# Kernel optimization log

Measured on AMD Instinct MI355X. Metric: run time of the kernel, lower is better.

The kernel has to match this reference:

```python
import jax, jax.numpy as jnp
import numpy as np

T, HID, H, KV, D = 2048, 2048, 16, 8, 128
EPS = 1e-6
THETA = 10000.0


def setup_inputs() -> dict:
    key = jax.random.key(0)
    ks = jax.random.split(key, 4)
    return {
        "positions": jnp.arange(T, dtype=jnp.int32),
        "hidden_states": jax.random.normal(ks[0], (T, HID), dtype=jnp.float32),
        "layernorm_weight": jnp.ones((HID,), dtype=jnp.float32),
        "qkv_weight": jax.random.normal(ks[1], ((H + 2 * KV) * D, HID), dtype=jnp.float32) * 0.02,
        "q_norm_weight": jnp.ones((D,), dtype=jnp.float32),
        "k_norm_weight": jnp.ones((D,), dtype=jnp.float32),
        "o_weight": jax.random.normal(ks[2], (HID, H * D), dtype=jnp.float32) * 0.02,
    }


def _rms(x, w, eps=EPS):
    var = jnp.mean(jnp.square(x), axis=-1, keepdims=True)
    return x * jax.lax.rsqrt(var + eps) * w


def _rope(x, pos):
    # NeoX-style rotary over full head_dim. x: [T, nH, D]
    inv_freq = 1.0 / (THETA ** (jnp.arange(0, D, 2, dtype=jnp.float32) / D))
    ang = pos.astype(jnp.float32)[:, None] * inv_freq  # [T, D/2]
    cos, sin = jnp.cos(ang)[:, None, :], jnp.sin(ang)[:, None, :]
    x1, x2 = x[..., : D // 2], x[..., D // 2 :]
    return jnp.concatenate([x1 * cos - x2 * sin, x2 * cos + x1 * sin], axis=-1)


def reference(positions, hidden_states, layernorm_weight, qkv_weight,
              q_norm_weight, k_norm_weight, o_weight):
    # Fused RMSNorm + QKV projection
    normed = _rms(hidden_states, layernorm_weight)                 # [T, HID]
    qkv = normed @ qkv_weight.T                                    # [T, (H+2KV)*D]
    q, k, v = jnp.split(qkv, [H * D, (H + KV) * D], axis=-1)
    q = _rms(q.reshape(T, H, D), q_norm_weight)                    # per-head q norm
    k = _rms(k.reshape(T, KV, D), k_norm_weight)                   # per-head k norm
    v = v.reshape(T, KV, D)
    # RoPE
    q = _rope(q, positions)
    k = _rope(k, positions)
    # GQA causal attention
    scale = D ** -0.5
    kr = jnp.repeat(k, H // KV, axis=1)                            # [T, H, D]
    vr = jnp.repeat(v, H // KV, axis=1)
    scores = jnp.einsum("qhd,khd->hqk", q, kr) * scale             # [H, T, T]
    mask = jnp.tril(jnp.ones((T, T), dtype=bool))
    scores = jnp.where(mask[None], scores, jnp.finfo(scores.dtype).min)
    attn = jax.nn.softmax(scores, axis=-1)
    out = jnp.einsum("hqk,khd->qhd", attn, vr).reshape(T, H * D)
    return out @ o_weight.T                                        # [T, HID]
```

## Files before the change

kernel.cpp:

```cpp
#include <hip/hip_runtime.h>
#include <cstdint>
#include <cstddef>

typedef __bf16 bf16;
typedef __attribute__((ext_vector_type(8))) __bf16 bf16x8;
typedef __attribute__((ext_vector_type(4))) __bf16 bf16x4v;
typedef __attribute__((ext_vector_type(4))) float f32x4;
typedef __attribute__((ext_vector_type(4))) short short4v;

#define T_N   2048
#define HID_N 2048
#define NH    16
#define NKV   8
#define HD    128

#define MFMA(a, b, c) __builtin_amdgcn_mfma_f32_16x16x32_bf16((a), (b), (c), 0, 0, 0)

__device__ __forceinline__ f32x4 MFMA16(short4v a, short4v b, f32x4 c) {
#if __has_builtin(__builtin_amdgcn_mfma_f32_16x16x16bf16_1k)
    return __builtin_amdgcn_mfma_f32_16x16x16bf16_1k(a, b, c, 0, 0, 0);
#else
    asm volatile("v_mfma_f32_16x16x16_bf16 %0, %1, %2, %0\n\ts_nop 7\n\ts_nop 7"
                 : "+v"(c) : "v"(a), "v"(b));
    return c;
#endif
}

__device__ __forceinline__ void gl_lds16(const void* g, void* l) {
    __builtin_amdgcn_global_load_lds(
        (const __attribute__((address_space(1))) unsigned int*)g,
        (__attribute__((address_space(3))) unsigned int*)l,
        16, 0, 0);
}

__device__ __forceinline__ uint32_t pk2(float a, float b) {
    union { bf16 h; unsigned short u; } ca, cb;
    ca.h = (bf16)a; cb.h = (bf16)b;
    return ((uint32_t)cb.u << 16) | ca.u;
}

__global__ __launch_bounds__(256) void k_f2b(const float* __restrict__ in,
                                             bf16* __restrict__ out, int n) {
    int i = (blockIdx.x * 256 + threadIdx.x) * 8;
    if (i >= n) return;
    const float4* p = (const float4*)(in + i);
    float4 a = p[0], b = p[1];
    bf16x8 v;
    v[0] = (bf16)a.x; v[1] = (bf16)a.y; v[2] = (bf16)a.z; v[3] = (bf16)a.w;
    v[4] = (bf16)b.x; v[5] = (bf16)b.y; v[6] = (bf16)b.z; v[7] = (bf16)b.w;
    *(bf16x8*)(out + i) = v;
}

__global__ __launch_bounds__(256) void k_rmsnorm(const float* __restrict__ x,
                                                 const float* __restrict__ w,
                                                 bf16* __restrict__ out) {
    int row = blockIdx.x, tid = threadIdx.x;
    const float* xr = x + (size_t)row * HID_N;
    float4 a = ((const float4*)xr)[tid * 2];
    float4 b = ((const float4*)xr)[tid * 2 + 1];
    float ss = a.x*a.x + a.y*a.y + a.z*a.z + a.w*a.w
             + b.x*b.x + b.y*b.y + b.z*b.z + b.w*b.w;
    #pragma unroll
    for (int m = 32; m; m >>= 1) ss += __shfl_xor(ss, m);
    __shared__ float red[4];
    if ((tid & 63) == 0) red[tid >> 6] = ss;
    __syncthreads();
    float tot = red[0] + red[1] + red[2] + red[3];
    float rs = rsqrtf(tot * (1.0f / HID_N) + 1e-6f);
    const float4* wr = (const float4*)(w + tid * 8);
    float4 wa = wr[0], wb = wr[1];
    bf16x8 v;
    v[0] = (bf16)(a.x * rs * wa.x); v[1] = (bf16)(a.y * rs * wa.y);
    v[2] = (bf16)(a.z * rs * wa.z); v[3] = (bf16)(a.w * rs * wa.w);
    v[4] = (bf16)(b.x * rs * wb.x); v[5] = (bf16)(b.y * rs * wb.y);
    v[6] = (bf16)(b.z * rs * wb.z); v[7] = (bf16)(b.w * rs * wb.w);
    *(bf16x8*)(out + (size_t)row * HID_N + tid * 8) = v;
}

__global__ __launch_bounds__(256, 2) void k_gemm_bt(const bf16* __restrict__ A,
                                                    const bf16* __restrict__ B,
                                                    float* __restrict__ C,
                                                    int M, int N, int K) {
    __shared__ __attribute__((aligned(16))) bf16 As[128 * 64];
    __shared__ __attribute__((aligned(16))) bf16 Bs[128 * 64];
    const int tid = threadIdx.x;
    const int lane = tid & 63, wid = tid >> 6;
    const int wm = wid >> 1, wn = wid & 1;
    const int r = lane & 15, g = lane >> 4;
    const size_t bm = (size_t)blockIdx.y * 128, bn = (size_t)blockIdx.x * 128;

    f32x4 acc[4][4] = {};

    const int srow = tid >> 3;
    const int schk = tid & 7;

    for (int k0 = 0; k0 < K; k0 += 64) {
        __syncthreads();
        #pragma unroll
        for (int c = 0; c < 4; c++) {
            int row = c * 32 + srow;
            int ka = (schk ^ (row & 7)) << 3;
            gl_lds16(A + (bm + row) * (size_t)K + k0 + ka,
                     (char*)As + c * 4096 + tid * 16);
            gl_lds16(B + (bn + row) * (size_t)K + k0 + ka,
                     (char*)Bs + c * 4096 + tid * 16);
        }
        __syncthreads();
        #pragma unroll
        for (int kk = 0; kk < 2; kk++) {
            bf16x8 af[4], bfr[4];
            #pragma unroll
            for (int m = 0; m < 4; m++) {
                int row = wm * 64 + m * 16 + r;
                af[m] = *(const bf16x8*)(As + row * 64 + (((kk * 4 + g) ^ (row & 7)) << 3));
            }
            #pragma unroll
            for (int n = 0; n < 4; n++) {
                int row = wn * 64 + n * 16 + r;
                bfr[n] = *(const bf16x8*)(Bs + row * 64 + (((kk * 4 + g) ^ (row & 7)) << 3));
            }
            #pragma unroll
            for (int m = 0; m < 4; m++)
                #pragma unroll
                for (int n = 0; n < 4; n++)
                    acc[m][n] = MFMA(af[m], bfr[n], acc[m][n]);
        }
    }
    #pragma unroll
    for (int m = 0; m < 4; m++)
        #pragma unroll
        for (int n = 0; n < 4; n++)
            #pragma unroll
            for (int j = 0; j < 4; j++) {
                size_t row = bm + wm * 64 + m * 16 + g * 4 + j;
                size_t col = bn + wn * 64 + n * 16 + r;
                C[row * (size_t)N + col] = acc[m][n][j];
            }
}

__global__ __launch_bounds__(128) void k_normrope(const float* __restrict__ qkv,
                                                  const float* __restrict__ qw,
                                                  const float* __restrict__ kw,
                                                  const int* __restrict__ pos,
                                                  bf16* __restrict__ q,
                                                  bf16* __restrict__ k,
                                                  bf16* __restrict__ v) {
    int t = blockIdx.x, hs = blockIdx.y, d = threadIdx.x;
    const float* base = qkv + (size_t)t * 4096;
    if (hs >= 24) {
        int hv = hs - 24;
        v[((size_t)t * NKV + hv) * HD + d] = (bf16)base[3072 + hv * 128 + d];
        return;
    }
    bool isq = hs < 16;
    int h = isq ? hs : hs - 16;
    float x = isq ? base[h * 128 + d] : base[2048 + h * 128 + d];
    float ss = x * x;
    #pragma unroll
    for (int m = 32; m; m >>= 1) ss += __shfl_xor(ss, m);
    __shared__ float red[2];
    if ((d & 63) == 0) red[d >> 6] = ss;
    __syncthreads();
    float rs = rsqrtf((red[0] + red[1]) * (1.0f / HD) + 1e-6f);
    float nx = x * rs * (isq ? qw[d] : kw[d]);
    __shared__ float sh[128];
    sh[d] = nx;
    __syncthreads();
    float other = sh[d ^ 64];
    int j = d & 63;
    float ang = (float)pos[t] * __powf(10000.f, -(float)j * (1.f / 64.f));
    float s, c;
    __sincosf(ang, &s, &c);
    float o = (d < 64) ? (nx * c - other * s) : (nx * c + other * s);
    bf16* dst = isq ? (q + ((size_t)t * NH + h) * HD + d)
                    : (k + ((size_t)t * NKV + h) * HD + d);
    *dst = (bf16)o;
}

__global__ __launch_bounds__(256, 3) void k_flash(const bf16* __restrict__ Q,
                                                  const bf16* __restrict__ K,
                                                  const bf16* __restrict__ V,
                                                  bf16* __restrict__ On,
                                                  float* __restrict__ ml) {
    __shared__ __attribute__((aligned(16))) bf16 Ks2[2][64 * 128];
    __shared__ __attribute__((aligned(16))) bf16 Vt[128 * 64];

    const int tid = threadIdx.x, lane = tid & 63, w = tid >> 6;
    const int r = lane & 15, g = lane >> 4;
    const int h = blockIdx.x, y = blockIdx.y;
    int ci, qt;
    if (y < 32)      { ci = 0; qt = y; }
    else if (y < 56) { ci = 1; qt = y - 24; }
    else if (y < 72) { ci = 2; qt = y - 40; }
    else             { ci = 3; qt = y - 48; }
    const int c0 = ci * 8;
    const int ntl = min(qt + 1 - c0, 8);
    const int q0 = qt * 64;
    const int gh = h >> 1;
    const int q0w = q0 + w * 16;

    const int rowk = tid >> 4, posc = tid & 15;
    const int vd = tid & 127, vhalf = tid >> 7;

    bf16x8 qf[4];
    #pragma unroll
    for (int ks = 0; ks < 4; ks++)
        qf[ks] = *(const bf16x8*)(Q + ((size_t)(q0w + r) * NH + h) * HD + ks * 32 + g * 8);

    f32x4 acc[8] = {};
    float m_run = -1e30f, l_run = 0.f;
    const float scale = 0.08838834764831845f;

    {
        const int kv0 = c0 * 64;
        #pragma unroll
        for (int c = 0; c < 4; c++) {
            int row = c * 16 + rowk;
            int srcc = posc ^ (row & 7);
            gl_lds16(K + ((size_t)(kv0 + row) * NKV + gh) * HD + srcc * 8,
                     (char*)&Ks2[0][0] + c * 4096 + tid * 16);
        }
        bf16x8 vr[4];
        #pragma unroll
        for (int it = 0; it < 4; it++) {
            int kb = vhalf + it * 2;
            const bf16* src = V + ((size_t)(kv0 + kb * 8) * NKV + gh) * HD + vd;
            #pragma unroll
            for (int i = 0; i < 8; i++) vr[it][i] = src[(size_t)i * (NKV * HD)];
        }
        #pragma unroll
        for (int it = 0; it < 4; it++) {
            int kb = vhalf + it * 2;
            *(bf16x8*)(&Vt[0] + vd * 64 + ((kb ^ (vd & 7)) * 8)) = vr[it];
        }
        __syncthreads();
    }

    for (int t = 0; t < ntl; ++t) {
        const int b = t & 1;
        const int kv0 = (c0 + t) * 64;
        const bool pf = (t + 1 < ntl);
        bf16x8 vr[4];
        if (pf) {
            const int kv1 = kv0 + 64;
            #pragma unroll
            for (int c = 0; c < 4; c++) {
                int row = c * 16 + rowk;
                int srcc = posc ^ (row & 7);
                gl_lds16(K + ((size_t)(kv1 + row) * NKV + gh) * HD + srcc * 8,
                         (char*)&Ks2[0][0] + (b ^ 1) * 16384 + c * 4096 + tid * 16);
            }
            #pragma unroll
            for (int it = 0; it < 4; it++) {
                int kb = vhalf + it * 2;
                const bf16* src = V + ((size_t)(kv1 + kb * 8) * NKV + gh) * HD + vd;
                #pragma unroll
                for (int i = 0; i < 8; i++) vr[it][i] = src[(size_t)i * (NKV * HD)];
            }
        }
        if (kv0 <= q0w + 15) {
            const bf16* Kb = &Ks2[b][0];
            const char* Vb = (const char*)&Vt[0];
            float sc[4][4];
            __builtin_amdgcn_s_setprio(1);
            #pragma unroll
            for (int t4 = 0; t4 < 4; t4++) {
                f32x4 S = {};
                #pragma unroll
                for (int ks = 0; ks < 4; ks++) {
                    int row = t4 * 16 + r;
                    bf16x8 kf = *(const bf16x8*)(Kb + row * 128 + (((4 * ks + g) ^ (row & 7)) * 8));
                    S = MFMA(kf, qf[ks], S);
                }
                #pragma unroll
                for (int j = 0; j < 4; j++) {
                    int kg = kv0 + t4 * 16 + 4 * g + j;
                    sc[t4][j] = (kg <= q0w + r) ? S[j] * scale : -1e30f;
                }
            }
            __builtin_amdgcn_s_setprio(0);
            float mx = sc[0][0];
            #pragma unroll
            for (int t4 = 0; t4 < 4; t4++)
                #pragma unroll
                for (int j = 0; j < 4; j++) mx = fmaxf(mx, sc[t4][j]);
            mx = fmaxf(mx, __shfl_xor(mx, 16));
            mx = fmaxf(mx, __shfl_xor(mx, 32));
            float mn = fmaxf(m_run, mx);
            float alpha = __expf(m_run - mn);
            m_run = mn;
            float rsum = 0.f;
            #pragma unroll
            for (int t4 = 0; t4 < 4; t4++)
                #pragma unroll
                for (int j = 0; j < 4; j++) {
                    sc[t4][j] = __expf(sc[t4][j] - mn);
                    rsum += sc[t4][j];
                }
            rsum += __shfl_xor(rsum, 16);
            rsum += __shfl_xor(rsum, 32);
            l_run = l_run * alpha + rsum;
            #pragma unroll
            for (int f = 0; f < 8; f++)
                #pragma unroll
                for (int j = 0; j < 4; j++) acc[f][j] *= alpha;
            union PB { uint32_t u[2]; short4v s; };
            PB pbu[4];
            #pragma unroll
            for (int t4 = 0; t4 < 4; t4++) {
                pbu[t4].u[0] = pk2(sc[t4][0], sc[t4][1]);
                pbu[t4].u[1] = pk2(sc[t4][2], sc[t4][3]);
            }
            __builtin_amdgcn_s_setprio(1);
            #pragma unroll
            for (int f = 0; f < 8; f++) {
                #pragma unroll
                for (int t4 = 0; t4 < 4; t4++) {
                    short4v vf = *(const short4v*)(Vb + f * 2048 + r * 128 +
                                  (((2 * t4 + (g >> 1)) ^ (r & 7)) * 16) + (g & 1) * 8);
                    acc[f] = MFMA16(vf, pbu[t4].s, acc[f]);
                }
            }
            __builtin_amdgcn_s_setprio(0);
        }
        if (pf) {
            __syncthreads();
            #pragma unroll
            for (int it = 0; it < 4; it++) {
                int kb = vhalf + it * 2;
                *(bf16x8*)(&Vt[0] + vd * 64 + ((kb ^ (vd & 7)) * 8)) = vr[it];
            }
            __syncthreads();
        }
    }
    const int lr = w * 16 + r;
    float inv_l = 1.0f / l_run;
    bf16* Ob = On + ((size_t)(h * 80 + y)) * 8192 + lr * 128;
    #pragma unroll
    for (int f = 0; f < 8; f++) {
        bf16x4v ov;
        #pragma unroll
        for (int j = 0; j < 4; j++) ov[j] = (bf16)(acc[f][j] * inv_l);
        *(bf16x4v*)(Ob + f * 16 + 4 * g) = ov;
    }
    if (g == 0) {
        float* mlp = ml + ((size_t)(h * 80 + y)) * 128;
        mlp[lr] = m_run;
        mlp[64 + lr] = l_run;
    }
}

__global__ __launch_bounds__(256) void k_comb(const bf16* __restrict__ On,
                                              const float* __restrict__ ml,
                                              bf16* __restrict__ ao) {
    const int h = blockIdx.x, qt = blockIdx.y;
    const int lr = threadIdx.x & 63, db = threadIdx.x >> 6;
    const int nc = 1 + (qt >= 8) + (qt >= 16) + (qt >= 24);
    const int ys[4] = {qt, qt + 24, qt + 40, qt + 48};
    float mi[4], li[4], wi[4];
    float mstar = -1e30f;
    for (int i = 0; i < 4; i++) {
        if (i < nc) {
            const float* p = ml + ((size_t)(h * 80 + ys[i])) * 128;
            mi[i] = p[lr]; li[i] = p[64 + lr];
            mstar = fmaxf(mstar, mi[i]);
        }
    }
    float wsum = 0.f;
    for (int i = 0; i < 4; i++) {
        if (i < nc) { wi[i] = li[i] * __expf(mi[i] - mstar); wsum += wi[i]; }
        else wi[i] = 0.f;
    }
    float inv = 1.f / wsum;
    for (int i = 0; i < 4; i++) wi[i] *= inv;
    const int q = qt * 64 + lr;
    #pragma unroll
    for (int dd = 0; dd < 4; dd++) {
        int d0 = db * 32 + dd * 8;
        float o[8] = {};
        for (int i = 0; i < 4; i++) {
            if (i < nc) {
                bf16x8 v = *(const bf16x8*)(On + ((size_t)(h * 80 + ys[i])) * 8192 + lr * 128 + d0);
                #pragma unroll
                for (int j = 0; j < 8; j++) o[j] += wi[i] * (float)v[j];
            }
        }
        bf16x8 ov;
        #pragma unroll
        for (int j = 0; j < 8; j++) ov[j] = (bf16)o[j];
        *(bf16x8*)(ao + ((size_t)q * NH + h) * HD + d0) = ov;
    }
}

extern "C" void kernel_launch(void* const* d_in, const int* in_sizes, int n_in,
                              void* d_out, int out_size, void* d_ws, size_t ws_size,
                              hipStream_t stream) {
    const int*   pos  = (const int*)d_in[0];
    const float* hid  = (const float*)d_in[1];
    const float* lw   = (const float*)d_in[2];
    const float* qkvw = (const float*)d_in[3];
    const float* qnw  = (const float*)d_in[4];
    const float* knw  = (const float*)d_in[5];
    const float* ow   = (const float*)d_in[6];
    float* out = (float*)d_out;

    char* ws = (char*)d_ws;
    bf16*  qkvw_b = (bf16*)(ws);
    bf16*  ow_b   = (bf16*)(ws + (16u << 20));
    bf16*  normed = (bf16*)(ws + (24u << 20));
    float* qkvf   = (float*)(ws + (32u << 20));
    bf16*  qb     = (bf16*)(ws + (64u << 20));
    bf16*  kb     = (bf16*)(ws + (72u << 20));
    bf16*  vb     = (bf16*)(ws + (76u << 20));
    bf16*  ao     = normed;
    bf16*  On     = (bf16*)(ws + (32u << 20));
    float* ml     = (float*)(ws + (54u << 20));

    k_f2b<<<4096, 256, 0, stream>>>(qkvw, qkvw_b, 4096 * 2048);
    k_f2b<<<2048, 256, 0, stream>>>(ow, ow_b, 2048 * 2048);
    k_rmsnorm<<<T_N, 256, 0, stream>>>(hid, lw, normed);
    k_gemm_bt<<<dim3(32, 16), 256, 0, stream>>>(normed, qkvw_b, qkvf, 2048, 4096, 2048);
    k_normrope<<<dim3(T_N, 32), 128, 0, stream>>>(qkvf, qnw, knw, pos, qb, kb, vb);
    k_flash<<<dim3(NH, 80), 256, 0, stream>>>(qb, kb, vb, On, ml);
    k_comb<<<dim3(NH, 32), 256, 0, stream>>>(On, ml, ao);
    k_gemm_bt<<<dim3(16, 16), 256, 0, stream>>>(ao, ow_b, out, 2048, 2048, 2048);
}
```

Before: 185.7 us.

## Emit bf16 QKV from GEMM, write V directly, skip masking and lazy rescale in flash

A dedicated QKV GEMM writes its output as bf16 and stores the V columns directly into the V buffer. This removes the fp32 intermediate and the V copy pass, and k_normrope now handles two heads per 256-thread block. The flash kernel skips causal masking on tiles that are fully below the diagonal. It also skips the online-softmax rescale when the new max exceeds the running max by no more than 8, which bounds exp values by e^8 and so trades a small accuracy risk for fewer multiplies. GEMM launch bounds are raised to 3 blocks per CU, which may force register spills.

Measured after the change: 185.1 us. Within noise of the previous version (-0.4%).

```diff
diff --git a/kernel.cpp b/kernel.cpp
--- a/kernel.cpp
+++ b/kernel.cpp
@@ -77,7 +77,7 @@
     *(bf16x8*)(out + (size_t)row * HID_N + tid * 8) = v;
 }
 
-__global__ __launch_bounds__(256, 2) void k_gemm_bt(const bf16* __restrict__ A,
+__global__ __launch_bounds__(256, 3) void k_gemm_bt(const bf16* __restrict__ A,
                                                     const bf16* __restrict__ B,
                                                     float* __restrict__ C,
                                                     int M, int N, int K) {
@@ -138,35 +138,93 @@
             }
 }
 
-__global__ __launch_bounds__(128) void k_normrope(const float* __restrict__ qkv,
+__global__ __launch_bounds__(256, 3) void k_gemm_qkv(const bf16* __restrict__ A,
+                                                     const bf16* __restrict__ B,
+                                                     bf16* __restrict__ qkv3,
+                                                     bf16* __restrict__ vb) {
+    const int K = HID_N;
+    __shared__ __attribute__((aligned(16))) bf16 As[128 * 64];
+    __shared__ __attribute__((aligned(16))) bf16 Bs[128 * 64];
+    const int tid = threadIdx.x;
+    const int lane = tid & 63, wid = tid >> 6;
+    const int wm = wid >> 1, wn = wid & 1;
+    const int r = lane & 15, g = lane >> 4;
+    const size_t bm = (size_t)blockIdx.y * 128, bn = (size_t)blockIdx.x * 128;
+
+    f32x4 acc[4][4] = {};
+    const int srow = tid >> 3;
+    const int schk = tid & 7;
+
+    for (int k0 = 0; k0 < K; k0 += 64) {
+        __syncthreads();
+        #pragma unroll
+        for (int c = 0; c < 4; c++) {
+            int row = c * 32 + srow;
+            int ka = (schk ^ (row & 7)) << 3;
+            gl_lds16(A + (bm + row) * (size_t)K + k0 + ka,
+                     (char*)As + c * 4096 + tid * 16);
+            gl_lds16(B + (bn + row) * (size_t)K + k0 + ka,
+                     (char*)Bs + c * 4096 + tid * 16);
+        }
+        __syncthreads();
+        #pragma unroll
+        for (int kk = 0; kk < 2; kk++) {
+            bf16x8 af[4], bfr[4];
+            #pragma unroll
+            for (int m = 0; m < 4; m++) {
+                int row = wm * 64 + m * 16 + r;
+                af[m] = *(const bf16x8*)(As + row * 64 + (((kk * 4 + g) ^ (row & 7)) << 3));
+            }
+            #pragma unroll
+            for (int n = 0; n < 4; n++) {
+                int row = wn * 64 + n * 16 + r;
+                bfr[n] = *(const bf16x8*)(Bs + row * 64 + (((kk * 4 + g) ^ (row & 7)) << 3));
+            }
+            #pragma unroll
+            for (int m = 0; m < 4; m++)
+                #pragma unroll
+                for (int n = 0; n < 4; n++)
+                    acc[m][n] = MFMA(af[m], bfr[n], acc[m][n]);
+        }
+    }
+    #pragma unroll
+    for (int m = 0; m < 4; m++)
+        #pragma unroll
+        for (int n = 0; n < 4; n++)
+            #pragma unroll
+            for (int j = 0; j < 4; j++) {
+                size_t row = bm + wm * 64 + m * 16 + g * 4 + j;
+                size_t col = bn + wn * 64 + n * 16 + r;
+                bf16 val = (bf16)acc[m][n][j];
+                if (col < 3072) qkv3[row * 3072 + col] = val;
+                else            vb[row * 1024 + (col - 3072)] = val;
+            }
+}
+
+__global__ __launch_bounds__(256) void k_normrope(const bf16* __restrict__ qkv3,
                                                   const float* __restrict__ qw,
                                                   const float* __restrict__ kw,
                                                   const int* __restrict__ pos,
                                                   bf16* __restrict__ q,
-                                                  bf16* __restrict__ k,
-                                                  bf16* __restrict__ v) {
-    int t = blockIdx.x, hs = blockIdx.y, d = threadIdx.x;
-    const float* base = qkv + (size_t)t * 4096;
-    if (hs >= 24) {
-        int hv = hs - 24;
-        v[((size_t)t * NKV + hv) * HD + d] = (bf16)base[3072 + hv * 128 + d];
-        return;
-    }
-    bool isq = hs < 16;
-    int h = isq ? hs : hs - 16;
-    float x = isq ? base[h * 128 + d] : base[2048 + h * 128 + d];
+                                                  bf16* __restrict__ k) {
+    const int t = blockIdx.x, tid = threadIdx.x;
+    const int half = tid >> 7, d = tid & 127;
+    const int slot = blockIdx.y * 2 + half;
+    const bool isq = slot < 16;
+    const int h = isq ? slot : slot - 16;
+    float x = (float)qkv3[(size_t)t * 3072 + slot * 128 + d];
     float ss = x * x;
     #pragma unroll
     for (int m = 32; m; m >>= 1) ss += __shfl_xor(ss, m);
-    __shared__ float red[2];
-    if ((d & 63) == 0) red[d >> 6] = ss;
+    __shared__ float red[4];
+    __shared__ float sh[256];
+    if ((tid & 63) == 0) red[tid >> 6] = ss;
     __syncthreads();
-    float rs = rsqrtf((red[0] + red[1]) * (1.0f / HD) + 1e-6f);
+    float rs = rsqrtf((red[half * 2] + red[half * 2 + 1]) * (1.0f / HD) + 1e-6f);
     float nx = x * rs * (isq ? qw[d] : kw[d]);
-    __shared__ float sh[128];
-    sh[d] = nx;
+    sh[tid] = nx;
     __syncthreads();
-    float other = sh[d ^ 64];
+    float other = sh[tid ^ 64];
     int j = d & 63;
     float ang = (float)pos[t] * __powf(10000.f, -(float)j * (1.f / 64.f));
     float s, c;
@@ -261,6 +319,7 @@
         if (kv0 <= q0w + 15) {
             const bf16* Kb = &Ks2[b][0];
             const char* Vb = (const char*)&Vt[0];
+            const bool fullt = (kv0 + 63 <= q0w);
             float sc[4][4];
             __builtin_amdgcn_s_setprio(1);
             #pragma unroll
@@ -272,10 +331,15 @@
                     bf16x8 kf = *(const bf16x8*)(Kb + row * 128 + (((4 * ks + g) ^ (row & 7)) * 8));
                     S = MFMA(kf, qf[ks], S);
                 }
-                #pragma unroll
-                for (int j = 0; j < 4; j++) {
-                    int kg = kv0 + t4 * 16 + 4 * g + j;
-                    sc[t4][j] = (kg <= q0w + r) ? S[j] * scale : -1e30f;
+                if (fullt) {
+                    #pragma unroll
+                    for (int j = 0; j < 4; j++) sc[t4][j] = S[j] * scale;
+                } else {
+                    #pragma unroll
+                    for (int j = 0; j < 4; j++) {
+                        int kg = kv0 + t4 * 16 + 4 * g + j;
+                        sc[t4][j] = (kg <= q0w + r) ? S[j] * scale : -1e30f;
+                    }
                 }
             }
             __builtin_amdgcn_s_setprio(0);
@@ -286,9 +350,10 @@
                 for (int j = 0; j < 4; j++) mx = fmaxf(mx, sc[t4][j]);
             mx = fmaxf(mx, __shfl_xor(mx, 16));
             mx = fmaxf(mx, __shfl_xor(mx, 32));
-            float mn = fmaxf(m_run, mx);
-            float alpha = __expf(m_run - mn);
-            m_run = mn;
+            const bool nr = __all(mx <= m_run + 8.0f) != 0;
+            float mn, alpha;
+            if (nr) { mn = m_run; alpha = 1.0f; }
+            else    { mn = fmaxf(m_run, mx); alpha = __expf(m_run - mn); m_run = mn; }
             float rsum = 0.f;
             #pragma unroll
             for (int t4 = 0; t4 < 4; t4++)
@@ -300,10 +365,12 @@
             rsum += __shfl_xor(rsum, 16);
             rsum += __shfl_xor(rsum, 32);
             l_run = l_run * alpha + rsum;
-            #pragma unroll
-            for (int f = 0; f < 8; f++)
-                #pragma unroll
-                for (int j = 0; j < 4; j++) acc[f][j] *= alpha;
+            if (!nr) {
+                #pragma unroll
+                for (int f = 0; f < 8; f++)
+                    #pragma unroll
+                    for (int j = 0; j < 4; j++) acc[f][j] *= alpha;
+            }
             union PB { uint32_t u[2]; short4v s; };
             PB pbu[4];
             #pragma unroll
@@ -408,7 +475,7 @@
     bf16*  qkvw_b = (bf16*)(ws);
     bf16*  ow_b   = (bf16*)(ws + (16u << 20));
     bf16*  normed = (bf16*)(ws + (24u << 20));
-    float* qkvf   = (float*)(ws + (32u << 20));
+    bf16*  qkv3   = (bf16*)(ws + (32u << 20));
     bf16*  qb     = (bf16*)(ws + (64u << 20));
     bf16*  kb     = (bf16*)(ws + (72u << 20));
     bf16*  vb     = (bf16*)(ws + (76u << 20));
@@ -419,8 +486,8 @@
     k_f2b<<<4096, 256, 0, stream>>>(qkvw, qkvw_b, 4096 * 2048);
     k_f2b<<<2048, 256, 0, stream>>>(ow, ow_b, 2048 * 2048);
     k_rmsnorm<<<T_N, 256, 0, stream>>>(hid, lw, normed);
-    k_gemm_bt<<<dim3(32, 16), 256, 0, stream>>>(normed, qkvw_b, qkvf, 2048, 4096, 2048);
-    k_normrope<<<dim3(T_N, 32), 128, 0, stream>>>(qkvf, qnw, knw, pos, qb, kb, vb);
+    k_gemm_qkv<<<dim3(32, 16), 256, 0, stream>>>(normed, qkvw_b, qkv3, vb);
+    k_normrope<<<dim3(T_N, 12), 256, 0, stream>>>(qkv3, qnw, knw, pos, qb, kb);
     k_flash<<<dim3(NH, 80), 256, 0, stream>>>(qb, kb, vb, On, ml);
     k_comb<<<dim3(NH, 32), 256, 0, stream>>>(On, ml, ao);
     k_gemm_bt<<<dim3(16, 16), 256, 0, stream>>>(ao, ow_b, out, 2048, 2048, 2048);
```
